# Kernel optimization log

Measured on AMD Instinct MI355X. Metric: run time of the kernel, lower is better.

Reference implementation:

```python
import jax, jax.numpy as jnp
import numpy as np

S, B, V, E, H, C = 512, 64, 50000, 300, 256, 5


def setup_inputs() -> dict:
    key = jax.random.key(0)
    ks = jax.random.split(key, 8)
    return {
        "inputs": jax.random.randint(ks[0], (S, B), 0, V, dtype=jnp.int64),
        "emb": jax.random.normal(ks[1], (V, E), dtype=jnp.float32),
        # small weight scale to keep tanh out of saturation (matches typical init scale)
        "W_ih": jax.random.normal(ks[2], (H, E), dtype=jnp.float32) * 0.05,
        "W_hh": jax.random.normal(ks[3], (H, H), dtype=jnp.float32) * 0.05,
        "b_ih": jax.random.normal(ks[4], (H,), dtype=jnp.float32) * 0.05,
        "b_hh": jax.random.normal(ks[5], (H,), dtype=jnp.float32) * 0.05,
        "W_out": jax.random.normal(ks[6], (C, H), dtype=jnp.float32) * 0.05,
        "b_out": jax.random.normal(ks[7], (C,), dtype=jnp.float32) * 0.05,
    }


def reference(inputs, emb, W_ih, W_hh, b_ih, b_hh, W_out, b_out):
    # embedding lookup: (S, B, E)
    x = emb[inputs]
    # precompute input-to-hidden projection for all timesteps: (S, B, H)
    xW = jnp.einsum("sbe,he->sbh", x, W_ih) + b_ih

    def step(h, xw_t):
        h_new = jnp.tanh(xw_t + h @ W_hh.T + b_hh)
        return h_new, h_new

    h0 = jnp.zeros((inputs.shape[1], W_hh.shape[0]), dtype=x.dtype)
    _, rnn_out = jax.lax.scan(step, h0, xW)  # (S, B, H)

    logits = jnp.einsum("sbh,ch->sbc", rnn_out, W_out) + b_out  # (S, B, C)
    summed = logits.sum(axis=0)  # (B, C)
    return jax.nn.log_softmax(summed, axis=1)
```

## Files before the change

### kernel.cpp

```cpp
#include <hip/hip_runtime.h>
#include <stdint.h>

#define S_ 512
#define B_ 64
#define V_ 50000
#define E_ 300
#define H_ 256
#define C_ 5
#define NPROD 248

typedef _Float16 h8_t __attribute__((ext_vector_type(8)));
typedef float f32x4 __attribute__((ext_vector_type(4)));

__device__ __forceinline__ float fast_tanh(float x) {
    float e = __builtin_amdgcn_exp2f(x * 2.88539008177793f);
    return fmaf(-2.0f, __builtin_amdgcn_rcpf(e + 1.0f), 1.0f);
}

__device__ __forceinline__ void wait_group(unsigned* gcnt, int grp) {
    while (__hip_atomic_load(&gcnt[grp], __ATOMIC_RELAXED,
                             __HIP_MEMORY_SCOPE_AGENT) != 64u) {
        __builtin_amdgcn_s_sleep(16);
    }
    __builtin_amdgcn_fence(__ATOMIC_ACQUIRE, "agent");
}

__device__ __forceinline__ h8_t load_wfrag(const float* __restrict__ W,
                                           int h, int e0) {
    h8_t v;
    if (e0 + 8 <= E_) {
        float4 f0 = *(const float4*)(W + (size_t)h * E_ + e0);
        float4 f1 = *(const float4*)(W + (size_t)h * E_ + e0 + 4);
        v[0] = (_Float16)f0.x; v[1] = (_Float16)f0.y;
        v[2] = (_Float16)f0.z; v[3] = (_Float16)f0.w;
        v[4] = (_Float16)f1.x; v[5] = (_Float16)f1.y;
        v[6] = (_Float16)f1.z; v[7] = (_Float16)f1.w;
    } else if (e0 < E_) {
        float4 f0 = *(const float4*)(W + (size_t)h * E_ + e0);
        v[0] = (_Float16)f0.x; v[1] = (_Float16)f0.y;
        v[2] = (_Float16)f0.z; v[3] = (_Float16)f0.w;
        v[4] = (_Float16)0.0f; v[5] = (_Float16)0.0f;
        v[6] = (_Float16)0.0f; v[7] = (_Float16)0.0f;
    } else {
        v = (h8_t)(_Float16)0.0f;
    }
    return v;
}

__global__ __launch_bounds__(512, 2) void fused_kernel(
    const int* __restrict__ idx, const float* __restrict__ emb,
    const float* __restrict__ W_ih, const float* __restrict__ b_ih,
    const float* __restrict__ b_hh, float* __restrict__ xw,
    const float* __restrict__ W_hh, const float* __restrict__ W_out,
    const float* __restrict__ b_out, float* __restrict__ out,
    unsigned* __restrict__ gcnt) {
    __shared__ __attribute__((aligned(16))) unsigned char smem[40960];
    const int tid = threadIdx.x;

    if (blockIdx.x >= 8) {
        const int p = blockIdx.x - 8;
        uint4* Afrag = (uint4*)smem;
        const int w = tid >> 6;
        const int l = tid & 63;
        const int n = l & 15;
        const int hi = l >> 4;

        h8_t bw0[10], bw1[10];
#pragma unroll
        for (int ks = 0; ks < 10; ++ks) {
            bw0[ks] = load_wfrag(W_ih, (2 * w) * 16 + n, ks * 32 + hi * 8);
            bw1[ks] = load_wfrag(W_ih, (2 * w + 1) * 16 + n, ks * 32 + hi * 8);
        }
        const float bias0 = b_ih[w * 32 + n] + b_hh[w * 32 + n];
        const float bias1 = b_ih[w * 32 + 16 + n] + b_hh[w * 32 + 16 + n];

        for (int s = p; s < S_; s += NPROD) {
            const int base = s * 64;
            __syncthreads();
            for (int cc = tid; cc < 64 * 40; cc += 512) {
                int m = cc / 40;
                int c = cc - m * 40;
                int ks = c >> 2;
                int hic = c & 3;
                const float* src = emb + (size_t)idx[base + m] * E_ + 8 * c;
                h8_t v;
                if (c < 37) {
                    float4 f0 = *(const float4*)src;
                    float4 f1 = *(const float4*)(src + 4);
                    v[0] = (_Float16)f0.x; v[1] = (_Float16)f0.y;
                    v[2] = (_Float16)f0.z; v[3] = (_Float16)f0.w;
                    v[4] = (_Float16)f1.x; v[5] = (_Float16)f1.y;
                    v[6] = (_Float16)f1.z; v[7] = (_Float16)f1.w;
                } else if (c == 37) {
                    float4 f0 = *(const float4*)src;
                    v[0] = (_Float16)f0.x; v[1] = (_Float16)f0.y;
                    v[2] = (_Float16)f0.z; v[3] = (_Float16)f0.w;
                    v[4] = (_Float16)0.0f; v[5] = (_Float16)0.0f;
                    v[6] = (_Float16)0.0f; v[7] = (_Float16)0.0f;
                } else {
                    v = (h8_t)(_Float16)0.0f;
                }
                int fl = (hic << 4) | (m & 15);
                int mt = m >> 4;
                Afrag[(mt * 10 + ks) * 64 + fl] = __builtin_bit_cast(uint4, v);
            }
            __syncthreads();

            f32x4 c[4][2];
#pragma unroll
            for (int mt = 0; mt < 4; ++mt) {
                c[mt][0] = (f32x4)bias0;
                c[mt][1] = (f32x4)bias1;
            }
#pragma unroll
            for (int ks = 0; ks < 10; ++ks) {
#pragma unroll
                for (int mt = 0; mt < 4; ++mt) {
                    h8_t a = __builtin_bit_cast(h8_t,
                                                Afrag[(mt * 10 + ks) * 64 + l]);
                    c[mt][0] = __builtin_amdgcn_mfma_f32_16x16x32_f16(
                        a, bw0[ks], c[mt][0], 0, 0, 0);
                    c[mt][1] = __builtin_amdgcn_mfma_f32_16x16x32_f16(
                        a, bw1[ks], c[mt][1], 0, 0, 0);
                }
            }
#pragma unroll
            for (int mt = 0; mt < 4; ++mt)
#pragma unroll
                for (int q = 0; q < 2; ++q) {
                    float* op = xw + (size_t)(base + mt * 16 + hi * 4) * H_ +
                                w * 32 + q * 16 + n;
#pragma unroll
                    for (int r = 0; r < 4; ++r)
                        op[(size_t)r * H_] = c[mt][q][r];
                }

            __syncthreads();
            if (tid == 0) {
                __threadfence();
                atomicAdd(&gcnt[s >> 6], 1u);
            }
        }
        return;
    }

    const int w = tid >> 6;
    const int l = tid & 63;
    const int n = l & 15;
    const int hi = l >> 4;
    const int col = n & 7;
    const int sel = n >> 3;
    const int bbase = blockIdx.x * 8;
    const int rowbase = w * 32;

    char* lds = (char*)smem;

    h8_t a[2][8];
#pragma unroll
    for (int mt = 0; mt < 2; ++mt) {
        const float* wr = W_hh + (size_t)(rowbase + mt * 16 + n) * H_;
#pragma unroll
        for (int ks = 0; ks < 8; ++ks) {
            const float* wp = wr + ks * 32 + hi * 8;
            float4 f0 = *(const float4*)wp;
            float4 f1 = *(const float4*)(wp + 4);
            h8_t v;
            v[0] = (_Float16)f0.x; v[1] = (_Float16)f0.y;
            v[2] = (_Float16)f0.z; v[3] = (_Float16)f0.w;
            v[4] = (_Float16)f1.x; v[5] = (_Float16)f1.y;
            v[6] = (_Float16)f1.z; v[7] = (_Float16)f1.w;
            a[mt][ks] = v;
        }
    }

    const int wboff =
        (w * 4 + sel * 2 + (hi >> 1)) * 128 + col * 16 + (hi & 1) * 8;
    const int rdbase = hi * 128 + col * 16;

    for (int t = tid; t < 1024; t += 512) ((unsigned int*)lds)[t] = 0u;

    f32x4 hs = (f32x4)0.0f;

    wait_group(gcnt, 0);

    const float* xwl = xw + (size_t)(bbase + col) * H_ + rowbase + hi * 4;
    f32x4 cv[4][2];
    cv[0][0] = *(const f32x4*)(xwl);
    cv[0][1] = *(const f32x4*)(xwl + 16);
    cv[1][0] = *(const f32x4*)(xwl + 16384);
    cv[1][1] = *(const f32x4*)(xwl + 16384 + 16);
    __syncthreads();

#define STEP(CUR, I, SBASE)                                                    \
    {                                                                          \
        int sp = (SBASE) + 2;                                                  \
        if (sp < S_ && (sp & 63) == 0) wait_group(gcnt, sp >> 6);              \
        if (sp > S_ - 1) sp = S_ - 1;                                          \
        cv[(I + 2) & 3][0] = *(const f32x4*)(xwl + (size_t)sp * 16384);        \
        cv[(I + 2) & 3][1] = *(const f32x4*)(xwl + (size_t)sp * 16384 + 16);   \
        h8_t bf[8];                                                            \
        _Pragma("unroll") for (int ks = 0; ks < 8; ++ks)                       \
            bf[ks] = *(const h8_t*)(lds + (CUR)*4096 + rdbase + ks * 512);     \
        _Pragma("unroll") for (int ks = 0; ks < 8; ++ks) {                     \
            cv[I][0] = __builtin_amdgcn_mfma_f32_16x16x32_f16(                 \
                a[0][ks], bf[ks], cv[I][0], 0, 0, 0);                          \
            cv[I][1] = __builtin_amdgcn_mfma_f32_16x16x32_f16(                 \
                a[1][ks], bf[ks], cv[I][1], 0, 0, 0);                          \
        }                                                                      \
        {                                                                      \
            f32x4 sv = (sel == 0) ? cv[I][0] : cv[I][1];                       \
            float h0 = fast_tanh(sv[0]);                                       \
            float h1 = fast_tanh(sv[1]);                                       \
            float h2 = fast_tanh(sv[2]);                                       \
            float h3 = fast_tanh(sv[3]);                                       \
            hs[0] += h0; hs[1] += h1; hs[2] += h2; hs[3] += h3;                \
            uint2 pk;                                                          \
            pk.x = __builtin_bit_cast(unsigned int,                            \
                                      __builtin_amdgcn_cvt_pkrtz(h0, h1));     \
            pk.y = __builtin_bit_cast(unsigned int,                            \
                                      __builtin_amdgcn_cvt_pkrtz(h2, h3));     \
            *(uint2*)(lds + ((CUR) ^ 1) * 4096 + wboff) = pk;                  \
        }                                                                      \
        asm volatile("s_waitcnt lgkmcnt(0)" ::: "memory");                     \
        __builtin_amdgcn_s_barrier();                                          \
    }

    for (int s = 0; s < S_; s += 4) {
        STEP(0, 0, s)
        STEP(1, 1, s + 1)
        STEP(0, 2, s + 2)
        STEP(1, 3, s + 3)
    }
#undef STEP

    {
        const int k0v = rowbase + sel * 16 + hi * 4;
        *(f32x4*)(lds + col * 1024 + k0v * 4) = hs;
    }
    __syncthreads();
    {
        const float* hrow = (const float*)(lds + w * 1024);
        float lg[C_];
#pragma unroll
        for (int c = 0; c < C_; ++c) {
            float p = 0.0f;
#pragma unroll
            for (int q = 0; q < 4; ++q)
                p = fmaf(hrow[l + 64 * q], W_out[c * H_ + l + 64 * q], p);
#pragma unroll
            for (int off = 32; off; off >>= 1) p += __shfl_xor(p, off);
            lg[c] = p + (float)S_ * b_out[c];
        }
        if (l == 0) {
            float m = lg[0];
#pragma unroll
            for (int c = 1; c < C_; ++c) m = fmaxf(m, lg[c]);
            float sum = 0.0f;
#pragma unroll
            for (int c = 0; c < C_; ++c) sum += expf(lg[c] - m);
            float lse = logf(sum);
#pragma unroll
            for (int c = 0; c < C_; ++c)
                out[(bbase + w) * C_ + c] = lg[c] - m - lse;
        }
    }
}

extern "C" void kernel_launch(void* const* d_in, const int* in_sizes, int n_in,
                              void* d_out, int out_size, void* d_ws,
                              size_t ws_size, hipStream_t stream) {
    const int* idx = (const int*)d_in[0];
    const float* emb = (const float*)d_in[1];
    const float* W_ih = (const float*)d_in[2];
    const float* W_hh = (const float*)d_in[3];
    const float* b_ih = (const float*)d_in[4];
    const float* b_hh = (const float*)d_in[5];
    const float* W_out = (const float*)d_in[6];
    const float* b_out = (const float*)d_in[7];
    float* out = (float*)d_out;

    float* ws = (float*)d_ws;
    float* xw = ws;
    unsigned* gcnt = (unsigned*)(xw + (size_t)S_ * B_ * H_);

    hipMemsetAsync(gcnt, 0, 8 * sizeof(unsigned), stream);
    hipLaunchKernelGGL(fused_kernel, dim3(8 + NPROD), dim3(512), 0, stream,
                       idx, emb, W_ih, b_ih, b_hh, xw, W_hh, W_out, b_out, out,
                       gcnt);
}
```

Before: 283.4 us.

## Split fused producer/consumer kernel into separate xW and RNN kernels

Replaces the single fused kernel, where 248 producer blocks computed the input projection while 8 RNN blocks spun on atomic group counters, with two sequential launches: a 512-block xW GEMM kernel and an 8-block recurrent kernel. This drops the memset, the atomic flag polling and the fences. It gives up the overlap between the projection and the early recurrence steps. It also splits the per-step MFMA accumulation into two independent chains, which shortens the dependent MFMA latency on the serial recurrence path.

```diff
diff --git a/kernel.cpp b/kernel.cpp
--- a/kernel.cpp
+++ b/kernel.cpp
@@ -7,7 +7,6 @@
 #define E_ 300
 #define H_ 256
 #define C_ 5
-#define NPROD 248
 
 typedef _Float16 h8_t __attribute__((ext_vector_type(8)));
 typedef float f32x4 __attribute__((ext_vector_type(4)));
@@ -15,14 +14,6 @@
 __device__ __forceinline__ float fast_tanh(float x) {
     float e = __builtin_amdgcn_exp2f(x * 2.88539008177793f);
     return fmaf(-2.0f, __builtin_amdgcn_rcpf(e + 1.0f), 1.0f);
-}
-
-__device__ __forceinline__ void wait_group(unsigned* gcnt, int grp) {
-    while (__hip_atomic_load(&gcnt[grp], __ATOMIC_RELAXED,
-                             __HIP_MEMORY_SCOPE_AGENT) != 64u) {
-        __builtin_amdgcn_s_sleep(16);
-    }
-    __builtin_amdgcn_fence(__ATOMIC_ACQUIRE, "agent");
 }
 
 __device__ __forceinline__ h8_t load_wfrag(const float* __restrict__ W,
@@ -47,103 +38,89 @@
     return v;
 }
 
-__global__ __launch_bounds__(512, 2) void fused_kernel(
+__global__ __launch_bounds__(512, 2) void xw_kernel(
     const int* __restrict__ idx, const float* __restrict__ emb,
     const float* __restrict__ W_ih, const float* __restrict__ b_ih,
-    const float* __restrict__ b_hh, float* __restrict__ xw,
-    const float* __restrict__ W_hh, const float* __restrict__ W_out,
-    const float* __restrict__ b_out, float* __restrict__ out,
-    unsigned* __restrict__ gcnt) {
-    __shared__ __attribute__((aligned(16))) unsigned char smem[40960];
+    const float* __restrict__ b_hh, float* __restrict__ xw) {
+    __shared__ uint4 Afrag[4 * 10 * 64];
     const int tid = threadIdx.x;
-
-    if (blockIdx.x >= 8) {
-        const int p = blockIdx.x - 8;
-        uint4* Afrag = (uint4*)smem;
-        const int w = tid >> 6;
-        const int l = tid & 63;
-        const int n = l & 15;
-        const int hi = l >> 4;
-
-        h8_t bw0[10], bw1[10];
-#pragma unroll
-        for (int ks = 0; ks < 10; ++ks) {
-            bw0[ks] = load_wfrag(W_ih, (2 * w) * 16 + n, ks * 32 + hi * 8);
-            bw1[ks] = load_wfrag(W_ih, (2 * w + 1) * 16 + n, ks * 32 + hi * 8);
-        }
-        const float bias0 = b_ih[w * 32 + n] + b_hh[w * 32 + n];
-        const float bias1 = b_ih[w * 32 + 16 + n] + b_hh[w * 32 + 16 + n];
-
-        for (int s = p; s < S_; s += NPROD) {
-            const int base = s * 64;
-            __syncthreads();
-            for (int cc = tid; cc < 64 * 40; cc += 512) {
-                int m = cc / 40;
-                int c = cc - m * 40;
-                int ks = c >> 2;
-                int hic = c & 3;
-                const float* src = emb + (size_t)idx[base + m] * E_ + 8 * c;
-                h8_t v;
-                if (c < 37) {
-                    float4 f0 = *(const float4*)src;
-                    float4 f1 = *(const float4*)(src + 4);
-                    v[0] = (_Float16)f0.x; v[1] = (_Float16)f0.y;
-                    v[2] = (_Float16)f0.z; v[3] = (_Float16)f0.w;
-                    v[4] = (_Float16)f1.x; v[5] = (_Float16)f1.y;
-                    v[6] = (_Float16)f1.z; v[7] = (_Float16)f1.w;
-                } else if (c == 37) {
-                    float4 f0 = *(const float4*)src;
-                    v[0] = (_Float16)f0.x; v[1] = (_Float16)f0.y;
-                    v[2] = (_Float16)f0.z; v[3] = (_Float16)f0.w;
-                    v[4] = (_Float16)0.0f; v[5] = (_Float16)0.0f;
-                    v[6] = (_Float16)0.0f; v[7] = (_Float16)0.0f;
-                } else {
-                    v = (h8_t)(_Float16)0.0f;
-                }
-                int fl = (hic << 4) | (m & 15);
-                int mt = m >> 4;
-                Afrag[(mt * 10 + ks) * 64 + fl] = __builtin_bit_cast(uint4, v);
-            }
-            __syncthreads();
-
-            f32x4 c[4][2];
-#pragma unroll
-            for (int mt = 0; mt < 4; ++mt) {
-                c[mt][0] = (f32x4)bias0;
-                c[mt][1] = (f32x4)bias1;
-            }
-#pragma unroll
-            for (int ks = 0; ks < 10; ++ks) {
-#pragma unroll
-                for (int mt = 0; mt < 4; ++mt) {
-                    h8_t a = __builtin_bit_cast(h8_t,
-                                                Afrag[(mt * 10 + ks) * 64 + l]);
-                    c[mt][0] = __builtin_amdgcn_mfma_f32_16x16x32_f16(
-                        a, bw0[ks], c[mt][0], 0, 0, 0);
-                    c[mt][1] = __builtin_amdgcn_mfma_f32_16x16x32_f16(
-                        a, bw1[ks], c[mt][1], 0, 0, 0);
-                }
-            }
-#pragma unroll
-            for (int mt = 0; mt < 4; ++mt)
-#pragma unroll
-                for (int q = 0; q < 2; ++q) {
-                    float* op = xw + (size_t)(base + mt * 16 + hi * 4) * H_ +
-                                w * 32 + q * 16 + n;
-#pragma unroll
-                    for (int r = 0; r < 4; ++r)
-                        op[(size_t)r * H_] = c[mt][q][r];
-                }
-
-            __syncthreads();
-            if (tid == 0) {
-                __threadfence();
-                atomicAdd(&gcnt[s >> 6], 1u);
-            }
-        }
-        return;
-    }
-
+    const int w = tid >> 6;
+    const int l = tid & 63;
+    const int n = l & 15;
+    const int hi = l >> 4;
+    const int base = blockIdx.x * 64;
+
+    h8_t bw0[10], bw1[10];
+#pragma unroll
+    for (int ks = 0; ks < 10; ++ks) {
+        bw0[ks] = load_wfrag(W_ih, (2 * w) * 16 + n, ks * 32 + hi * 8);
+        bw1[ks] = load_wfrag(W_ih, (2 * w + 1) * 16 + n, ks * 32 + hi * 8);
+    }
+    const float bias0 = b_ih[w * 32 + n] + b_hh[w * 32 + n];
+    const float bias1 = b_ih[w * 32 + 16 + n] + b_hh[w * 32 + 16 + n];
+
+    for (int cc = tid; cc < 64 * 40; cc += 512) {
+        int m = cc / 40;
+        int c = cc - m * 40;
+        int ks = c >> 2;
+        int hic = c & 3;
+        const float* src = emb + (size_t)idx[base + m] * E_ + 8 * c;
+        h8_t v;
+        if (c < 37) {
+            float4 f0 = *(const float4*)src;
+            float4 f1 = *(const float4*)(src + 4);
+            v[0] = (_Float16)f0.x; v[1] = (_Float16)f0.y;
+            v[2] = (_Float16)f0.z; v[3] = (_Float16)f0.w;
+            v[4] = (_Float16)f1.x; v[5] = (_Float16)f1.y;
+            v[6] = (_Float16)f1.z; v[7] = (_Float16)f1.w;
+        } else if (c == 37) {
+            float4 f0 = *(const float4*)src;
+            v[0] = (_Float16)f0.x; v[1] = (_Float16)f0.y;
+            v[2] = (_Float16)f0.z; v[3] = (_Float16)f0.w;
+            v[4] = (_Float16)0.0f; v[5] = (_Float16)0.0f;
+            v[6] = (_Float16)0.0f; v[7] = (_Float16)0.0f;
+        } else {
+            v = (h8_t)(_Float16)0.0f;
+        }
+        int fl = (hic << 4) | (m & 15);
+        int mt = m >> 4;
+        Afrag[(mt * 10 + ks) * 64 + fl] = __builtin_bit_cast(uint4, v);
+    }
+    __syncthreads();
+
+    f32x4 c[4][2];
+#pragma unroll
+    for (int mt = 0; mt < 4; ++mt) {
+        c[mt][0] = (f32x4)bias0;
+        c[mt][1] = (f32x4)bias1;
+    }
+#pragma unroll
+    for (int ks = 0; ks < 10; ++ks) {
+#pragma unroll
+        for (int mt = 0; mt < 4; ++mt) {
+            h8_t a = __builtin_bit_cast(h8_t, Afrag[(mt * 10 + ks) * 64 + l]);
+            c[mt][0] = __builtin_amdgcn_mfma_f32_16x16x32_f16(a, bw0[ks],
+                                                              c[mt][0], 0, 0, 0);
+            c[mt][1] = __builtin_amdgcn_mfma_f32_16x16x32_f16(a, bw1[ks],
+                                                              c[mt][1], 0, 0, 0);
+        }
+    }
+#pragma unroll
+    for (int mt = 0; mt < 4; ++mt)
+#pragma unroll
+        for (int q = 0; q < 2; ++q) {
+            float* op =
+                xw + (size_t)(base + mt * 16 + hi * 4) * H_ + w * 32 + q * 16 + n;
+#pragma unroll
+            for (int r = 0; r < 4; ++r) op[(size_t)r * H_] = c[mt][q][r];
+        }
+}
+
+__global__ __launch_bounds__(512, 2) void rnn_kernel(
+    const float* __restrict__ xw, const float* __restrict__ W_hh,
+    const float* __restrict__ W_out, const float* __restrict__ b_out,
+    float* __restrict__ out) {
+    const int tid = threadIdx.x;
     const int w = tid >> 6;
     const int l = tid & 63;
     const int n = l & 15;
@@ -153,6 +130,7 @@
     const int bbase = blockIdx.x * 8;
     const int rowbase = w * 32;
 
+    __shared__ __attribute__((aligned(16))) unsigned char smem[8192];
     char* lds = (char*)smem;
 
     h8_t a[2][8];
@@ -181,8 +159,6 @@
 
     f32x4 hs = (f32x4)0.0f;
 
-    wait_group(gcnt, 0);
-
     const float* xwl = xw + (size_t)(bbase + col) * H_ + rowbase + hi * 4;
     f32x4 cv[4][2];
     cv[0][0] = *(const f32x4*)(xwl);
@@ -194,21 +170,28 @@
 #define STEP(CUR, I, SBASE)                                                    \
     {                                                                          \
         int sp = (SBASE) + 2;                                                  \
-        if (sp < S_ && (sp & 63) == 0) wait_group(gcnt, sp >> 6);              \
         if (sp > S_ - 1) sp = S_ - 1;                                          \
         cv[(I + 2) & 3][0] = *(const f32x4*)(xwl + (size_t)sp * 16384);        \
         cv[(I + 2) & 3][1] = *(const f32x4*)(xwl + (size_t)sp * 16384 + 16);   \
         h8_t bf[8];                                                            \
         _Pragma("unroll") for (int ks = 0; ks < 8; ++ks)                       \
             bf[ks] = *(const h8_t*)(lds + (CUR)*4096 + rdbase + ks * 512);     \
-        _Pragma("unroll") for (int ks = 0; ks < 8; ++ks) {                     \
-            cv[I][0] = __builtin_amdgcn_mfma_f32_16x16x32_f16(                 \
-                a[0][ks], bf[ks], cv[I][0], 0, 0, 0);                          \
-            cv[I][1] = __builtin_amdgcn_mfma_f32_16x16x32_f16(                 \
-                a[1][ks], bf[ks], cv[I][1], 0, 0, 0);                          \
+        f32x4 c0a = cv[I][0], c1a = cv[I][1];                                  \
+        f32x4 c0b = (f32x4)0.0f, c1b = (f32x4)0.0f;                            \
+        _Pragma("unroll") for (int ks = 0; ks < 4; ++ks) {                     \
+            c0a = __builtin_amdgcn_mfma_f32_16x16x32_f16(a[0][ks], bf[ks],     \
+                                                         c0a, 0, 0, 0);        \
+            c1a = __builtin_amdgcn_mfma_f32_16x16x32_f16(a[1][ks], bf[ks],     \
+                                                         c1a, 0, 0, 0);        \
+            c0b = __builtin_amdgcn_mfma_f32_16x16x32_f16(                      \
+                a[0][ks + 4], bf[ks + 4], c0b, 0, 0, 0);                       \
+            c1b = __builtin_amdgcn_mfma_f32_16x16x32_f16(                      \
+                a[1][ks + 4], bf[ks + 4], c1b, 0, 0, 0);                       \
         }                                                                      \
         {                                                                      \
-            f32x4 sv = (sel == 0) ? cv[I][0] : cv[I][1];                       \
+            f32x4 sva = (sel == 0) ? c0a : c1a;                                \
+            f32x4 svb = (sel == 0) ? c0b : c1b;                                \
+            f32x4 sv = sva + svb;                                              \
             float h0 = fast_tanh(sv[0]);                                       \
             float h1 = fast_tanh(sv[1]);                                       \
             float h2 = fast_tanh(sv[2]);                                       \
@@ -279,12 +262,10 @@
     const float* b_out = (const float*)d_in[7];
     float* out = (float*)d_out;
 
-    float* ws = (float*)d_ws;
-    float* xw = ws;
-    unsigned* gcnt = (unsigned*)(xw + (size_t)S_ * B_ * H_);
-
-    hipMemsetAsync(gcnt, 0, 8 * sizeof(unsigned), stream);
-    hipLaunchKernelGGL(fused_kernel, dim3(8 + NPROD), dim3(512), 0, stream,
-                       idx, emb, W_ih, b_ih, b_hh, xw, W_hh, W_out, b_out, out,
-                       gcnt);
-}
+    float* xw = (float*)d_ws;
+
+    hipLaunchKernelGGL(xw_kernel, dim3((S_ * B_) / 64), dim3(512), 0, stream,
+                       idx, emb, W_ih, b_ih, b_hh, xw);
+    hipLaunchKernelGGL(rnn_kernel, dim3(8), dim3(512), 0, stream, xw, W_hh,
+                       W_out, b_out, out);
+}
```

New measurement: 272.4 us. 1.04x faster.
